# Kernel tuning notes

Measured on AMD Instinct MI355X. Metric: run time of the kernel, lower is better.

The kernel has to match this reference:

```python
import jax, jax.numpy as jnp
import numpy as np

B, L, K, D = 32, 1024, 1024, 1024

def setup_inputs() -> dict:
    key = jax.random.key(0)
    k1, k2, k3, k4, k5 = jax.random.split(key, 5)
    query = jax.random.normal(k1, (B, L, D), dtype=jnp.float32)
    context = jax.random.normal(k2, (B, K, D), dtype=jnp.float32)
    mask = jax.random.randint(k3, (B * L, K), 0, 2, dtype=jnp.int32)
    W_in = jax.random.normal(k4, (D, D), dtype=jnp.float32) * (D ** -0.5)
    W_out = jax.random.normal(k5, (D, 2 * D), dtype=jnp.float32) * ((2 * D) ** -0.5)
    return {"query": query, "context": context, "mask": mask, "W_in": W_in, "W_out": W_out}

def reference(query, context, mask, W_in, W_out):
    b, l, d = query.shape
    k = context.shape[1]
    # linear_in (general attention): q @ W_in.T
    q = jnp.einsum('bld,ed->ble', query, W_in)
    # attention scores [b, l, k]
    scores = jnp.einsum('bld,bkd->blk', q, context)
    # multiplicative-mask softmax with renormalization (masked_softmax, non-memory-efficient path)
    m = mask.astype(scores.dtype).reshape(b, l, k)
    w = jax.nn.softmax(scores * m, axis=-1) * m
    w = w / (jnp.sum(w, axis=-1, keepdims=True) + 1e-13)
    # mix attended context, concat with transformed query, project, tanh
    mix = jnp.einsum('blk,bkd->bld', w, context)
    combined = jnp.concatenate([mix, q], axis=-1)          # [b, l, 2d]
    out = jnp.tanh(jnp.einsum('blc,dc->bld', combined, W_out))
    return out
```

## Files before the change

kernel.cpp:

```cpp
#include <hip/hip_runtime.h>
#include <math.h>

typedef __bf16 bf16_t;
typedef __bf16 bf16x4 __attribute__((ext_vector_type(4)));
typedef __bf16 bf16x8 __attribute__((ext_vector_type(8)));
typedef _Float16 f16x4 __attribute__((ext_vector_type(4)));
typedef _Float16 f16x8 __attribute__((ext_vector_type(8)));
typedef float f32x4 __attribute__((ext_vector_type(4)));
typedef int i32x4 __attribute__((ext_vector_type(4)));

#define MFMA_BF16 __builtin_amdgcn_mfma_f32_16x16x32_bf16
#define MFMA_F16  __builtin_amdgcn_mfma_f32_16x16x32_f16


__device__ __forceinline__ bf16_t to_bf16_rne(float x, float& rep) {
    unsigned u = __builtin_bit_cast(unsigned, x);
    unsigned r = u + 0x7fffu + ((u >> 16) & 1u);
    unsigned short h = (unsigned short)(r >> 16);
    rep = __builtin_bit_cast(float, ((unsigned)h) << 16);
    return __builtin_bit_cast(bf16_t, h);
}

__device__ __forceinline__ void g2l16(const void* g, void* l) {
    __builtin_amdgcn_global_load_lds(
        (const __attribute__((address_space(1))) unsigned int*)g,
        (__attribute__((address_space(3))) unsigned int*)l, 16, 0, 0);
}

__device__ __forceinline__ int lch(int r, int j) {
    return (r * 8 + (j ^ (r & 7))) * 8;
}

template <typename T>
__device__ __forceinline__ void stage2(const T* __restrict__ gA, long long ldA,
                                       const T* __restrict__ gB, long long ldB,
                                       T* buf, int tid) {
    int wid = tid >> 6, lane = tid & 63;
#pragma unroll
    for (int i = 0; i < 4; ++i) {
        int cb = i * 512 + wid * 64;
        int c = cb + lane;
        int r = c >> 3, j = (c & 7) ^ (r & 7);
        g2l16(gA + (long long)r * ldA + j * 8, buf + (size_t)cb * 8);
    }
#pragma unroll
    for (int i = 0; i < 4; ++i) {
        int cb = i * 512 + wid * 64;
        int c = cb + lane;
        int r = c >> 3, j = (c & 7) ^ (r & 7);
        g2l16(gB + (long long)r * ldB + j * 8, buf + 16384 + (size_t)cb * 8);
    }
}


__global__ __launch_bounds__(256) void split_int_k(const float* __restrict__ in,
                                                   bf16_t* __restrict__ out,
                                                   long long n4) {
    long long i = (long long)blockIdx.x * 256 + threadIdx.x;
    if (i >= n4) return;
    f32x4 v = ((const f32x4*)in)[i];
    bf16x4 hv, lv;
#pragma unroll
    for (int j = 0; j < 4; ++j) {
        float rep;
        hv[j] = to_bf16_rne(v[j], rep);
        float res = v[j] - rep;
        float rep2;
        lv[j] = to_bf16_rne(res, rep2);
    }
    long long row = i >> 8;
    int k = (int)(i & 255) * 4;
    long long base = row * 2048 + ((k >> 5) << 6) + (k & 31);
    *(bf16x4*)(out + base) = hv;
    *(bf16x4*)(out + base + 32) = lv;
}

__global__ __launch_bounds__(256) void cast_f16_k(const float* __restrict__ in,
                                                  _Float16* __restrict__ o, long long n4) {
    long long i = (long long)blockIdx.x * 256 + threadIdx.x;
    if (i >= n4) return;
    f32x4 v = ((const f32x4*)in)[i];
    f16x4 h;
#pragma unroll
    for (int j = 0; j < 4; ++j) h[j] = (_Float16)v[j];
    ((f16x4*)o)[i] = h;
}

__global__ __launch_bounds__(256) void prep_ctx_k(const float* __restrict__ ctx,
                                                  bf16_t* __restrict__ ctx_int,
                                                  _Float16* __restrict__ ctxT) {
    __shared__ _Float16 tl[32][33];
    int b = blockIdx.z;
    int k0 = blockIdx.x * 32, d0 = blockIdx.y * 32;
    const float* src = ctx + ((long long)b * 1024 + k0) * 1024 + d0;
    int x = threadIdx.x, y = threadIdx.y;
#pragma unroll
    for (int i = 0; i < 4; ++i) {
        int k = y + i * 8;
        float v = src[(long long)k * 1024 + x];
        float rep;
        bf16_t hb = to_bf16_rne(v, rep);
        float rep2;
        bf16_t lb = to_bf16_rne(v - rep, rep2);
        long long rb = ((long long)b * 1024 + k0 + k) * 2048 + d0 * 2 + x;
        ctx_int[rb] = hb;
        ctx_int[rb + 32] = lb;
        tl[x][k] = (_Float16)v;
    }
    __syncthreads();
    _Float16* dst = ctxT + ((long long)b * 1024 + d0) * 1024 + k0;
#pragma unroll
    for (int i = 0; i < 4; ++i) {
        int dd = y + i * 8;
        dst[(long long)dd * 1024 + x] = tl[dd][x];
    }
}

__global__ __launch_bounds__(256) void masked_softmax_k(const float* __restrict__ s,
                                                        const int* __restrict__ m,
                                                        _Float16* __restrict__ w) {
    long long row = blockIdx.x;
    const f32x4* sr = (const f32x4*)(s + row * 1024);
    const i32x4* mr = (const i32x4*)(m + row * 1024);
    f16x4* wr_ = (f16x4*)(w + row * 1024);
    int t = threadIdx.x;
    int lane = t & 63, wid = t >> 6;
    f32x4 v = sr[t];
    i32x4 mk = mr[t];
    float mx = -3.0e38f;
#pragma unroll
    for (int i = 0; i < 4; ++i)
        if (mk[i]) mx = fmaxf(mx, v[i]);
#pragma unroll
    for (int off = 32; off; off >>= 1) mx = fmaxf(mx, __shfl_xor(mx, off));
    __shared__ float rm[4], rs[4];
    if (!lane) rm[wid] = mx;
    __syncthreads();
    mx = fmaxf(fmaxf(rm[0], rm[1]), fmaxf(rm[2], rm[3]));
    float sum = 0.f;
    f32x4 e;
#pragma unroll
    for (int i = 0; i < 4; ++i) {
        e[i] = mk[i] ? expf(v[i] - mx) : 0.f;
        sum += e[i];
    }
#pragma unroll
    for (int off = 32; off; off >>= 1) sum += __shfl_xor(sum, off);
    if (!lane) rs[wid] = sum;
    __syncthreads();
    sum = rs[0] + rs[1] + rs[2] + rs[3];
    float inv = sum > 0.f ? 1.0f / sum : 0.f;
    f16x4 o;
#pragma unroll
    for (int i = 0; i < 4; ++i) o[i] = (_Float16)(e[i] * inv);
    wr_[t] = o;
}

template <int EPI>
__global__ __launch_bounds__(512, 2) void gemm_x3_256(
    const bf16_t* __restrict__ Aint, const bf16_t* __restrict__ Bint,
    long long sA, long long sB, long long sC, int nbx, int nby,
    float* __restrict__ Cs, bf16_t* __restrict__ Qint, _Float16* __restrict__ Qf) {
    __shared__ bf16_t lds[65536];
    const int NT = 32;
    int tid = threadIdx.x, lane = tid & 63, wid = tid >> 6;
    int wr = wid >> 2, wc = wid & 3;
    int nwg = gridDim.x;
    int bid = blockIdx.x;
    int lid = (bid & 7) * (nwg >> 3) + (bid >> 3);
    int by = lid % nby;
    int t2 = lid / nby;
    int bx = t2 % nbx;
    int z = t2 / nbx;
    const bf16_t* At = Aint + (long long)z * sA + (long long)bx * 256 * 2048;
    const bf16_t* Bt = Bint + (long long)z * sB + (long long)by * 256 * 2048;
    stage2(At, 2048ll, Bt, 2048ll, lds, tid);
    stage2(At + 64, 2048ll, Bt + 64, 2048ll, lds + 32768, tid);
    f32x4 acc[8][4] = {};
    for (int t = 0; t < NT; ++t) {
        bf16_t* buf = lds + (size_t)(t & 1) * 32768;
        bf16_t* bufB = buf + 16384;
        if (t < NT - 1) {
            asm volatile("s_waitcnt vmcnt(8)" ::: "memory");
        } else {
            asm volatile("s_waitcnt vmcnt(0)" ::: "memory");
        }
        __builtin_amdgcn_sched_barrier(0);
        __builtin_amdgcn_s_barrier();
        __builtin_amdgcn_sched_barrier(0);
        bf16x8 bh[4], bl[4];
#pragma unroll
        for (int n = 0; n < 4; ++n) {
            int rB = wc * 64 + n * 16 + (lane & 15);
            bh[n] = *(const bf16x8*)(bufB + lch(rB, lane >> 4));
            bl[n] = *(const bf16x8*)(bufB + lch(rB, 4 + (lane >> 4)));
        }
#pragma unroll
        for (int p = 0; p < 3; ++p) {
            bf16x8 ah[2], al[2];
#pragma unroll
            for (int i = 0; i < 2; ++i) {
                int rA = wr * 128 + (p * 2 + i) * 16 + (lane & 15);
                ah[i] = *(const bf16x8*)(buf + lch(rA, lane >> 4));
                al[i] = *(const bf16x8*)(buf + lch(rA, 4 + (lane >> 4)));
            }
            __builtin_amdgcn_s_setprio(1);
#pragma unroll
            for (int i = 0; i < 2; ++i)
#pragma unroll
                for (int n = 0; n < 4; ++n) {
                    f32x4 a = acc[p * 2 + i][n];
                    a = MFMA_BF16(ah[i], bh[n], a, 0, 0, 0);
                    a = MFMA_BF16(ah[i], bl[n], a, 0, 0, 0);
                    a = MFMA_BF16(al[i], bh[n], a, 0, 0, 0);
                    acc[p * 2 + i][n] = a;
                }
            __builtin_amdgcn_s_setprio(0);
        }
        bf16x8 ah3[2], al3[2];
#pragma unroll
        for (int i = 0; i < 2; ++i) {
            int rA = wr * 128 + (6 + i) * 16 + (lane & 15);
            ah3[i] = *(const bf16x8*)(buf + lch(rA, lane >> 4));
            al3[i] = *(const bf16x8*)(buf + lch(rA, 4 + (lane >> 4)));
        }
        asm volatile("s_waitcnt lgkmcnt(0)" ::: "memory");
        __builtin_amdgcn_sched_barrier(0);
        __builtin_amdgcn_s_barrier();
        __builtin_amdgcn_sched_barrier(0);
        if (t + 2 < NT)
            stage2(At + (long long)(t + 2) * 64, 2048ll, Bt + (long long)(t + 2) * 64,
                   2048ll, buf, tid);
        __builtin_amdgcn_s_setprio(1);
#pragma unroll
        for (int i = 0; i < 2; ++i)
#pragma unroll
            for (int n = 0; n < 4; ++n) {
                f32x4 a = acc[6 + i][n];
                a = MFMA_BF16(ah3[i], bh[n], a, 0, 0, 0);
                a = MFMA_BF16(ah3[i], bl[n], a, 0, 0, 0);
                a = MFMA_BF16(al3[i], bh[n], a, 0, 0, 0);
                acc[6 + i][n] = a;
            }
        __builtin_amdgcn_s_setprio(0);
    }
    int r0 = bx * 256 + wr * 128 + ((lane >> 4) << 2);
    int c0 = by * 256 + wc * 64 + (lane & 15);
#pragma unroll
    for (int m = 0; m < 8; ++m)
#pragma unroll
        for (int n = 0; n < 4; ++n)
#pragma unroll
            for (int j = 0; j < 4; ++j) {
                int r = r0 + m * 16 + j;
                int c = c0 + n * 16;
                float v = acc[m][n][j];
                if (EPI == 0) {
                    Cs[(long long)z * sC + (long long)r * 1024 + c] = v;
                } else {
                    float rep;
                    bf16_t hb = to_bf16_rne(v, rep);
                    float res = v - rep;
                    float rep2;
                    bf16_t lb = to_bf16_rne(res, rep2);
                    long long rb = (long long)r * 2048 + ((c >> 5) << 6) + (c & 31);
                    Qint[rb] = hb;
                    Qint[rb + 32] = lb;
                    Qf[(long long)r * 1024 + c] = (_Float16)v;
                }
            }
}

template <int EPI>
__global__ __launch_bounds__(512, 2) void gemm_f16_256(
    const _Float16* __restrict__ A1, const _Float16* __restrict__ A2,
    const _Float16* __restrict__ B,
    long long ldA, long long ldB, long long sA, long long sB, long long sC,
    int NT, int swt, int nbx, int nby,
    _Float16* __restrict__ Cm, float* __restrict__ Co) {
    __shared__ _Float16 lds[65536];
    int tid = threadIdx.x, lane = tid & 63, wid = tid >> 6;
    int wr = wid >> 2, wc = wid & 3;
    int nwg = gridDim.x;
    int bid = blockIdx.x;
    int lid = (bid & 7) * (nwg >> 3) + (bid >> 3);
    int by = lid % nby;
    int t2 = lid / nby;
    int bx = t2 % nbx;
    int z = t2 / nbx;
    const _Float16* A1t = A1 + (long long)z * sA + (long long)bx * 256 * ldA;
    const _Float16* A2t = A2 + (long long)bx * 256 * ldA;
    const _Float16* Bt = B + (long long)z * sB + (long long)by * 256 * ldB;
    stage2((0 < swt) ? A1t : A2t, ldA, Bt, ldB, lds, tid);
    stage2((1 < swt) ? A1t + 64 : A2t + (long long)(1 - swt) * 64, ldA, Bt + 64, ldB,
           lds + 32768, tid);
    f32x4 acc[8][4] = {};
    for (int t = 0; t < NT; ++t) {
        _Float16* buf = lds + (size_t)(t & 1) * 32768;
        _Float16* bufB = buf + 16384;
        if (t < NT - 1) {
            asm volatile("s_waitcnt vmcnt(8)" ::: "memory");
        } else {
            asm volatile("s_waitcnt vmcnt(0)" ::: "memory");
        }
        __builtin_amdgcn_sched_barrier(0);
        __builtin_amdgcn_s_barrier();
        __builtin_amdgcn_sched_barrier(0);
        f16x8 bfr[4][2];
#pragma unroll
        for (int n = 0; n < 4; ++n)
#pragma unroll
            for (int ks = 0; ks < 2; ++ks) {
                int rB = wc * 64 + n * 16 + (lane & 15);
                bfr[n][ks] = *(const f16x8*)(bufB + lch(rB, ks * 4 + (lane >> 4)));
            }
#pragma unroll
        for (int p = 0; p < 3; ++p) {
            f16x8 a[2][2];
#pragma unroll
            for (int i = 0; i < 2; ++i)
#pragma unroll
                for (int ks = 0; ks < 2; ++ks) {
                    int rA = wr * 128 + (p * 2 + i) * 16 + (lane & 15);
                    a[i][ks] = *(const f16x8*)(buf + lch(rA, ks * 4 + (lane >> 4)));
                }
            __builtin_amdgcn_s_setprio(1);
#pragma unroll
            for (int i = 0; i < 2; ++i)
#pragma unroll
                for (int n = 0; n < 4; ++n) {
                    f32x4 v = acc[p * 2 + i][n];
                    v = MFMA_F16(a[i][0], bfr[n][0], v, 0, 0, 0);
                    v = MFMA_F16(a[i][1], bfr[n][1], v, 0, 0, 0);
                    acc[p * 2 + i][n] = v;
                }
            __builtin_amdgcn_s_setprio(0);
        }
        f16x8 a3[2][2];
#pragma unroll
        for (int i = 0; i < 2; ++i)
#pragma unroll
            for (int ks = 0; ks < 2; ++ks) {
                int rA = wr * 128 + (6 + i) * 16 + (lane & 15);
                a3[i][ks] = *(const f16x8*)(buf + lch(rA, ks * 4 + (lane >> 4)));
            }
        asm volatile("s_waitcnt lgkmcnt(0)" ::: "memory");
        __builtin_amdgcn_sched_barrier(0);
        __builtin_amdgcn_s_barrier();
        __builtin_amdgcn_sched_barrier(0);
        if (t + 2 < NT) {
            int tt = t + 2;
            const _Float16* gA =
                (tt < swt) ? A1t + (long long)tt * 64 : A2t + (long long)(tt - swt) * 64;
            stage2(gA, ldA, Bt + (long long)tt * 64, ldB,
                   lds + (size_t)(tt & 1) * 32768, tid);
        }
        __builtin_amdgcn_s_setprio(1);
#pragma unroll
        for (int i = 0; i < 2; ++i)
#pragma unroll
            for (int n = 0; n < 4; ++n) {
                f32x4 v = acc[6 + i][n];
                v = MFMA_F16(a3[i][0], bfr[n][0], v, 0, 0, 0);
                v = MFMA_F16(a3[i][1], bfr[n][1], v, 0, 0, 0);
                acc[6 + i][n] = v;
            }
        __builtin_amdgcn_s_setprio(0);
    }
    int r0 = bx * 256 + wr * 128 + ((lane >> 4) << 2);
    int c0 = by * 256 + wc * 64 + (lane & 15);
#pragma unroll
    for (int m = 0; m < 8; ++m)
#pragma unroll
        for (int n = 0; n < 4; ++n)
#pragma unroll
            for (int j = 0; j < 4; ++j) {
                int r = r0 + m * 16 + j;
                int c = c0 + n * 16;
                float v = acc[m][n][j];
                if (EPI == 0) {
                    Cm[(long long)z * sC + (long long)r * 1024 + c] = (_Float16)v;
                } else {
                    Co[(long long)r * 1024 + c] = tanhf(v);
                }
            }
}


extern "C" void kernel_launch(void* const* d_in, const int* in_sizes, int n_in,
                              void* d_out, int out_size, void* d_ws, size_t ws_size,
                              hipStream_t stream) {
    const float* query = (const float*)d_in[0];
    const float* ctx = (const float*)d_in[1];
    const int* mask = (const int*)d_in[2];
    const float* Win = (const float*)d_in[3];
    const float* Wout = (const float*)d_in[4];
    float* outp = (float*)d_out;

    const long long MB = 1048576ll;
    int G = 1;
    if ((long long)ws_size >= 512 * MB) G = 32;
    else if ((long long)ws_size >= 256 * MB) G = 16;
    else if ((long long)ws_size >= 128 * MB) G = 8;
    else if ((long long)ws_size >= 64 * MB) G = 4;
    else if ((long long)ws_size >= 32 * MB) G = 2;

    char* p = (char*)d_ws;
    const long long R = (long long)G * 1024;
    bf16_t* qint = (bf16_t*)p; p += 4 * G * MB;
    _Float16* qf = (_Float16*)p; p += 2 * G * MB;
    char* slabA = p; p += 4 * G * MB;
    bf16_t* win_int = (bf16_t*)slabA;
    bf16_t* ctx_int = (bf16_t*)slabA;
    _Float16* wf = (_Float16*)slabA;
    _Float16* mixf = (_Float16*)(slabA + 2 * G * MB);
    _Float16* ctxT = (_Float16*)p; p += 2 * G * MB;
    char* slabC = p;
    bf16_t* qs_int = (bf16_t*)slabC;
    float* scores = (float*)slabC;
    _Float16* woutf = (_Float16*)slabC;

    const long long LD = 1048576ll;

    for (int b0 = 0; b0 < 32; b0 += G) {
        const float* qsrc = query + (long long)b0 * LD;
        const float* csrc = ctx + (long long)b0 * LD;
        split_int_k<<<1024, 256, 0, stream>>>(Win, win_int, 262144ll);
        split_int_k<<<(int)R, 256, 0, stream>>>(qsrc, qs_int, R * 256);
        gemm_x3_256<1><<<16 * G, 512, 0, stream>>>(
            qs_int, win_int, 0, 0, 0, 4 * G, 4, nullptr, qint, qf);
        prep_ctx_k<<<dim3(32, 32, G), dim3(32, 8, 1), 0, stream>>>(csrc, ctx_int, ctxT);
        gemm_x3_256<0><<<16 * G, 512, 0, stream>>>(
            qint, ctx_int, 2097152ll, 2097152ll, 1048576ll, 4, 4,
            scores, nullptr, nullptr);
        masked_softmax_k<<<(int)R, 256, 0, stream>>>(
            scores, mask + (long long)b0 * 1024 * 1024, wf);
        cast_f16_k<<<2048, 256, 0, stream>>>(Wout, woutf, 524288ll);
        gemm_f16_256<0><<<16 * G, 512, 0, stream>>>(
            wf, wf, ctxT, 1024ll, 1024ll, 1048576ll, 1048576ll, 1048576ll,
            16, 1 << 20, 4, 4, mixf, nullptr);
        gemm_f16_256<1><<<16 * G, 512, 0, stream>>>(
            mixf, qf, woutf, 1024ll, 2048ll, 0, 0, 0,
            32, 16, 4 * G, 4, nullptr, outp + (long long)b0 * LD);
    }
}
```

Measured before the change: 778.8 us.

## Restructure GEMM main loops into barrier-fenced phases with split A/B prefetch

Result: faster. 762.3 us (median of 2 runs) (-2.1%).

```diff
diff --git a/kernel.cpp b/kernel.cpp
--- a/kernel.cpp
+++ b/kernel.cpp
@@ -12,6 +12,17 @@
 #define MFMA_BF16 __builtin_amdgcn_mfma_f32_16x16x32_bf16
 #define MFMA_F16  __builtin_amdgcn_mfma_f32_16x16x32_f16
 
+#define P_PRE                                         \
+    __builtin_amdgcn_sched_barrier(0);                \
+    __builtin_amdgcn_s_barrier();                     \
+    asm volatile("s_waitcnt lgkmcnt(0)" ::: "memory");\
+    __builtin_amdgcn_sched_barrier(0);                \
+    __builtin_amdgcn_s_setprio(1)
+#define P_POST                                        \
+    __builtin_amdgcn_s_setprio(0);                    \
+    __builtin_amdgcn_sched_barrier(0);                \
+    __builtin_amdgcn_s_barrier()
+
 
 __device__ __forceinline__ bf16_t to_bf16_rne(float x, float& rep) {
     unsigned u = __builtin_bit_cast(unsigned, x);
@@ -32,9 +43,8 @@
 }
 
 template <typename T>
-__device__ __forceinline__ void stage2(const T* __restrict__ gA, long long ldA,
-                                       const T* __restrict__ gB, long long ldB,
-                                       T* buf, int tid) {
+__device__ __forceinline__ void stageA4(const T* __restrict__ gA, long long ldA,
+                                        T* buf, int tid) {
     int wid = tid >> 6, lane = tid & 63;
 #pragma unroll
     for (int i = 0; i < 4; ++i) {
@@ -43,6 +53,12 @@
         int r = c >> 3, j = (c & 7) ^ (r & 7);
         g2l16(gA + (long long)r * ldA + j * 8, buf + (size_t)cb * 8);
     }
+}
+
+template <typename T>
+__device__ __forceinline__ void stageB4(const T* __restrict__ gB, long long ldB,
+                                        T* buf, int tid) {
+    int wid = tid >> 6, lane = tid & 63;
 #pragma unroll
     for (int i = 0; i < 4; ++i) {
         int cb = i * 512 + wid * 64;
@@ -50,6 +66,14 @@
         int r = c >> 3, j = (c & 7) ^ (r & 7);
         g2l16(gB + (long long)r * ldB + j * 8, buf + 16384 + (size_t)cb * 8);
     }
+}
+
+template <typename T>
+__device__ __forceinline__ void stage2(const T* __restrict__ gA, long long ldA,
+                                       const T* __restrict__ gB, long long ldB,
+                                       T* buf, int tid) {
+    stageA4(gA, ldA, buf, tid);
+    stageB4(gB, ldB, buf, tid);
 }
 
 
@@ -169,83 +193,118 @@
     int bid = blockIdx.x;
     int lid = (bid & 7) * (nwg >> 3) + (bid >> 3);
     int by = lid % nby;
-    int t2 = lid / nby;
-    int bx = t2 % nbx;
-    int z = t2 / nbx;
+    int t2_ = lid / nby;
+    int bx = t2_ % nbx;
+    int z = t2_ / nbx;
     const bf16_t* At = Aint + (long long)z * sA + (long long)bx * 256 * 2048;
     const bf16_t* Bt = Bint + (long long)z * sB + (long long)by * 256 * 2048;
     stage2(At, 2048ll, Bt, 2048ll, lds, tid);
     stage2(At + 64, 2048ll, Bt + 64, 2048ll, lds + 32768, tid);
     f32x4 acc[8][4] = {};
+    int l15 = lane & 15, l4 = lane >> 4;
+    asm volatile("s_waitcnt vmcnt(8)" ::: "memory");
+    __builtin_amdgcn_sched_barrier(0);
+    __builtin_amdgcn_s_barrier();
     for (int t = 0; t < NT; ++t) {
         bf16_t* buf = lds + (size_t)(t & 1) * 32768;
         bf16_t* bufB = buf + 16384;
-        if (t < NT - 1) {
+        const bf16_t* At2 = At + (long long)(t + 2) * 64;
+        const bf16_t* Bt2 = Bt + (long long)(t + 2) * 64;
+        bool st = (t + 2 < NT);
+        bf16x8 bh[4], bl[4], ahA[2], alA[2];
+#pragma unroll
+        for (int n = 0; n < 4; ++n) {
+            int rB = wc * 64 + n * 16 + l15;
+            bh[n] = *(const bf16x8*)(bufB + lch(rB, l4));
+            bl[n] = *(const bf16x8*)(bufB + lch(rB, 4 + l4));
+        }
+#pragma unroll
+        for (int i = 0; i < 2; ++i) {
+            int rA = wr * 128 + i * 16 + l15;
+            ahA[i] = *(const bf16x8*)(buf + lch(rA, l4));
+            alA[i] = *(const bf16x8*)(buf + lch(rA, 4 + l4));
+        }
+        P_PRE;
+#pragma unroll
+        for (int i = 0; i < 2; ++i)
+#pragma unroll
+            for (int n = 0; n < 4; ++n) {
+                f32x4 a = acc[i][n];
+                a = MFMA_BF16(ahA[i], bh[n], a, 0, 0, 0);
+                a = MFMA_BF16(ahA[i], bl[n], a, 0, 0, 0);
+                a = MFMA_BF16(alA[i], bh[n], a, 0, 0, 0);
+                acc[i][n] = a;
+            }
+        P_POST;
+        bf16x8 ahB[2], alB[2], ahC[2], alC[2];
+#pragma unroll
+        for (int i = 0; i < 2; ++i) {
+            int rA = wr * 128 + (2 + i) * 16 + l15;
+            ahB[i] = *(const bf16x8*)(buf + lch(rA, l4));
+            alB[i] = *(const bf16x8*)(buf + lch(rA, 4 + l4));
+        }
+#pragma unroll
+        for (int i = 0; i < 2; ++i) {
+            int rA = wr * 128 + (4 + i) * 16 + l15;
+            ahC[i] = *(const bf16x8*)(buf + lch(rA, l4));
+            alC[i] = *(const bf16x8*)(buf + lch(rA, 4 + l4));
+        }
+        P_PRE;
+#pragma unroll
+        for (int i = 0; i < 2; ++i)
+#pragma unroll
+            for (int n = 0; n < 4; ++n) {
+                f32x4 a = acc[2 + i][n];
+                a = MFMA_BF16(ahB[i], bh[n], a, 0, 0, 0);
+                a = MFMA_BF16(ahB[i], bl[n], a, 0, 0, 0);
+                a = MFMA_BF16(alB[i], bh[n], a, 0, 0, 0);
+                acc[2 + i][n] = a;
+            }
+        P_POST;
+        bf16x8 ahD[2], alD[2];
+#pragma unroll
+        for (int i = 0; i < 2; ++i) {
+            int rA = wr * 128 + (6 + i) * 16 + l15;
+            ahD[i] = *(const bf16x8*)(buf + lch(rA, l4));
+            alD[i] = *(const bf16x8*)(buf + lch(rA, 4 + l4));
+        }
+        if (st) stageB4(Bt2, 2048ll, buf, tid);
+        P_PRE;
+#pragma unroll
+        for (int i = 0; i < 2; ++i)
+#pragma unroll
+            for (int n = 0; n < 4; ++n) {
+                f32x4 a = acc[4 + i][n];
+                a = MFMA_BF16(ahC[i], bh[n], a, 0, 0, 0);
+                a = MFMA_BF16(ahC[i], bl[n], a, 0, 0, 0);
+                a = MFMA_BF16(alC[i], bh[n], a, 0, 0, 0);
+                acc[4 + i][n] = a;
+            }
+        P_POST;
+        if (st) stageA4(At2, 2048ll, buf, tid);
+        __builtin_amdgcn_s_setprio(1);
+#pragma unroll
+        for (int i = 0; i < 2; ++i)
+#pragma unroll
+            for (int n = 0; n < 4; ++n) {
+                f32x4 a = acc[6 + i][n];
+                a = MFMA_BF16(ahD[i], bh[n], a, 0, 0, 0);
+                a = MFMA_BF16(ahD[i], bl[n], a, 0, 0, 0);
+                a = MFMA_BF16(alD[i], bh[n], a, 0, 0, 0);
+                acc[6 + i][n] = a;
+            }
+        __builtin_amdgcn_s_setprio(0);
+        __builtin_amdgcn_sched_barrier(0);
+        if (t + 2 < NT) {
             asm volatile("s_waitcnt vmcnt(8)" ::: "memory");
-        } else {
+        } else if (t + 1 < NT) {
             asm volatile("s_waitcnt vmcnt(0)" ::: "memory");
         }
         __builtin_amdgcn_sched_barrier(0);
         __builtin_amdgcn_s_barrier();
-        __builtin_amdgcn_sched_barrier(0);
-        bf16x8 bh[4], bl[4];
-#pragma unroll
-        for (int n = 0; n < 4; ++n) {
-            int rB = wc * 64 + n * 16 + (lane & 15);
-            bh[n] = *(const bf16x8*)(bufB + lch(rB, lane >> 4));
-            bl[n] = *(const bf16x8*)(bufB + lch(rB, 4 + (lane >> 4)));
-        }
-#pragma unroll
-        for (int p = 0; p < 3; ++p) {
-            bf16x8 ah[2], al[2];
-#pragma unroll
-            for (int i = 0; i < 2; ++i) {
-                int rA = wr * 128 + (p * 2 + i) * 16 + (lane & 15);
-                ah[i] = *(const bf16x8*)(buf + lch(rA, lane >> 4));
-                al[i] = *(const bf16x8*)(buf + lch(rA, 4 + (lane >> 4)));
-            }
-            __builtin_amdgcn_s_setprio(1);
-#pragma unroll
-            for (int i = 0; i < 2; ++i)
-#pragma unroll
-                for (int n = 0; n < 4; ++n) {
-                    f32x4 a = acc[p * 2 + i][n];
-                    a = MFMA_BF16(ah[i], bh[n], a, 0, 0, 0);
-                    a = MFMA_BF16(ah[i], bl[n], a, 0, 0, 0);
-                    a = MFMA_BF16(al[i], bh[n], a, 0, 0, 0);
-                    acc[p * 2 + i][n] = a;
-                }
-            __builtin_amdgcn_s_setprio(0);
-        }
-        bf16x8 ah3[2], al3[2];
-#pragma unroll
-        for (int i = 0; i < 2; ++i) {
-            int rA = wr * 128 + (6 + i) * 16 + (lane & 15);
-            ah3[i] = *(const bf16x8*)(buf + lch(rA, lane >> 4));
-            al3[i] = *(const bf16x8*)(buf + lch(rA, 4 + (lane >> 4)));
-        }
-        asm volatile("s_waitcnt lgkmcnt(0)" ::: "memory");
-        __builtin_amdgcn_sched_barrier(0);
-        __builtin_amdgcn_s_barrier();
-        __builtin_amdgcn_sched_barrier(0);
-        if (t + 2 < NT)
-            stage2(At + (long long)(t + 2) * 64, 2048ll, Bt + (long long)(t + 2) * 64,
-                   2048ll, buf, tid);
-        __builtin_amdgcn_s_setprio(1);
-#pragma unroll
-        for (int i = 0; i < 2; ++i)
-#pragma unroll
-            for (int n = 0; n < 4; ++n) {
-                f32x4 a = acc[6 + i][n];
-                a = MFMA_BF16(ah3[i], bh[n], a, 0, 0, 0);
-                a = MFMA_BF16(ah3[i], bl[n], a, 0, 0, 0);
-                a = MFMA_BF16(al3[i], bh[n], a, 0, 0, 0);
-                acc[6 + i][n] = a;
-            }
-        __builtin_amdgcn_s_setprio(0);
-    }
-    int r0 = bx * 256 + wr * 128 + ((lane >> 4) << 2);
-    int c0 = by * 256 + wc * 64 + (lane & 15);
+    }
+    int r0 = bx * 256 + wr * 128 + (l4 << 2);
+    int c0 = by * 256 + wc * 64 + l15;
 #pragma unroll
     for (int m = 0; m < 8; ++m)
 #pragma unroll
@@ -285,9 +344,9 @@
     int bid = blockIdx.x;
     int lid = (bid & 7) * (nwg >> 3) + (bid >> 3);
     int by = lid % nby;
-    int t2 = lid / nby;
-    int bx = t2 % nbx;
-    int z = t2 / nbx;
+    int t2_ = lid / nby;
+    int bx = t2_ % nbx;
+    int z = t2_ / nbx;
     const _Float16* A1t = A1 + (long long)z * sA + (long long)bx * 256 * ldA;
     const _Float16* A2t = A2 + (long long)bx * 256 * ldA;
     const _Float16* Bt = B + (long long)z * sB + (long long)by * 256 * ldB;
@@ -295,80 +354,113 @@
     stage2((1 < swt) ? A1t + 64 : A2t + (long long)(1 - swt) * 64, ldA, Bt + 64, ldB,
            lds + 32768, tid);
     f32x4 acc[8][4] = {};
+    int l15 = lane & 15, l4 = lane >> 4;
+    asm volatile("s_waitcnt vmcnt(8)" ::: "memory");
+    __builtin_amdgcn_sched_barrier(0);
+    __builtin_amdgcn_s_barrier();
     for (int t = 0; t < NT; ++t) {
         _Float16* buf = lds + (size_t)(t & 1) * 32768;
         _Float16* bufB = buf + 16384;
-        if (t < NT - 1) {
+        int tt = t + 2;
+        bool st = (tt < NT);
+        const _Float16* gA2 =
+            (tt < swt) ? A1t + (long long)tt * 64 : A2t + (long long)(tt - swt) * 64;
+        const _Float16* gB2 = Bt + (long long)tt * 64;
+        f16x8 bfr[4][2], aA[2][2];
+#pragma unroll
+        for (int n = 0; n < 4; ++n) {
+            int rB = wc * 64 + n * 16 + l15;
+#pragma unroll
+            for (int ks = 0; ks < 2; ++ks)
+                bfr[n][ks] = *(const f16x8*)(bufB + lch(rB, ks * 4 + l4));
+        }
+#pragma unroll
+        for (int i = 0; i < 2; ++i) {
+            int rA = wr * 128 + i * 16 + l15;
+#pragma unroll
+            for (int ks = 0; ks < 2; ++ks)
+                aA[i][ks] = *(const f16x8*)(buf + lch(rA, ks * 4 + l4));
+        }
+        P_PRE;
+#pragma unroll
+        for (int i = 0; i < 2; ++i)
+#pragma unroll
+            for (int n = 0; n < 4; ++n) {
+                f32x4 v = acc[i][n];
+                v = MFMA_F16(aA[i][0], bfr[n][0], v, 0, 0, 0);
+                v = MFMA_F16(aA[i][1], bfr[n][1], v, 0, 0, 0);
+                acc[i][n] = v;
+            }
+        P_POST;
+        f16x8 aB[2][2], aC[2][2];
+#pragma unroll
+        for (int i = 0; i < 2; ++i) {
+            int rA = wr * 128 + (2 + i) * 16 + l15;
+#pragma unroll
+            for (int ks = 0; ks < 2; ++ks)
+                aB[i][ks] = *(const f16x8*)(buf + lch(rA, ks * 4 + l4));
+        }
+#pragma unroll
+        for (int i = 0; i < 2; ++i) {
+            int rA = wr * 128 + (4 + i) * 16 + l15;
+#pragma unroll
+            for (int ks = 0; ks < 2; ++ks)
+                aC[i][ks] = *(const f16x8*)(buf + lch(rA, ks * 4 + l4));
+        }
+        P_PRE;
+#pragma unroll
+        for (int i = 0; i < 2; ++i)
+#pragma unroll
+            for (int n = 0; n < 4; ++n) {
+                f32x4 v = acc[2 + i][n];
+                v = MFMA_F16(aB[i][0], bfr[n][0], v, 0, 0, 0);
+                v = MFMA_F16(aB[i][1], bfr[n][1], v, 0, 0, 0);
+                acc[2 + i][n] = v;
+            }
+        P_POST;
+        f16x8 aD[2][2];
+#pragma unroll
+        for (int i = 0; i < 2; ++i) {
+            int rA = wr * 128 + (6 + i) * 16 + l15;
+#pragma unroll
+            for (int ks = 0; ks < 2; ++ks)
+                aD[i][ks] = *(const f16x8*)(buf + lch(rA, ks * 4 + l4));
+        }
+        if (st) stageB4(gB2, ldB, buf, tid);
+        P_PRE;
+#pragma unroll
+        for (int i = 0; i < 2; ++i)
+#pragma unroll
+            for (int n = 0; n < 4; ++n) {
+                f32x4 v = acc[4 + i][n];
+                v = MFMA_F16(aC[i][0], bfr[n][0], v, 0, 0, 0);
+                v = MFMA_F16(aC[i][1], bfr[n][1], v, 0, 0, 0);
+                acc[4 + i][n] = v;
+            }
+        P_POST;
+        if (st) stageA4(gA2, ldA, buf, tid);
+        __builtin_amdgcn_s_setprio(1);
+#pragma unroll
+        for (int i = 0; i < 2; ++i)
+#pragma unroll
+            for (int n = 0; n < 4; ++n) {
+                f32x4 v = acc[6 + i][n];
+                v = MFMA_F16(aD[i][0], bfr[n][0], v, 0, 0, 0);
+                v = MFMA_F16(aD[i][1], bfr[n][1], v, 0, 0, 0);
+                acc[6 + i][n] = v;
+            }
+        __builtin_amdgcn_s_setprio(0);
+        __builtin_amdgcn_sched_barrier(0);
+        if (t + 2 < NT) {
             asm volatile("s_waitcnt vmcnt(8)" ::: "memory");
-        } else {
+        } else if (t + 1 < NT) {
             asm volatile("s_waitcnt vmcnt(0)" ::: "memory");
         }
         __builtin_amdgcn_sched_barrier(0);
         __builtin_amdgcn_s_barrier();
-        __builtin_amdgcn_sched_barrier(0);
-        f16x8 bfr[4][2];
-#pragma unroll
-        for (int n = 0; n < 4; ++n)
-#pragma unroll
-            for (int ks = 0; ks < 2; ++ks) {
-                int rB = wc * 64 + n * 16 + (lane & 15);
-                bfr[n][ks] = *(const f16x8*)(bufB + lch(rB, ks * 4 + (lane >> 4)));
-            }
-#pragma unroll
-        for (int p = 0; p < 3; ++p) {
-            f16x8 a[2][2];
-#pragma unroll
-            for (int i = 0; i < 2; ++i)
-#pragma unroll
-                for (int ks = 0; ks < 2; ++ks) {
-                    int rA = wr * 128 + (p * 2 + i) * 16 + (lane & 15);
-                    a[i][ks] = *(const f16x8*)(buf + lch(rA, ks * 4 + (lane >> 4)));
-                }
-            __builtin_amdgcn_s_setprio(1);
-#pragma unroll
-            for (int i = 0; i < 2; ++i)
-#pragma unroll
-                for (int n = 0; n < 4; ++n) {
-                    f32x4 v = acc[p * 2 + i][n];
-                    v = MFMA_F16(a[i][0], bfr[n][0], v, 0, 0, 0);
-                    v = MFMA_F16(a[i][1], bfr[n][1], v, 0, 0, 0);
-                    acc[p * 2 + i][n] = v;
-                }
-            __builtin_amdgcn_s_setprio(0);
-        }
-        f16x8 a3[2][2];
-#pragma unroll
-        for (int i = 0; i < 2; ++i)
-#pragma unroll
-            for (int ks = 0; ks < 2; ++ks) {
-                int rA = wr * 128 + (6 + i) * 16 + (lane & 15);
-                a3[i][ks] = *(const f16x8*)(buf + lch(rA, ks * 4 + (lane >> 4)));
-            }
-        asm volatile("s_waitcnt lgkmcnt(0)" ::: "memory");
-        __builtin_amdgcn_sched_barrier(0);
-        __builtin_amdgcn_s_barrier();
-        __builtin_amdgcn_sched_barrier(0);
-        if (t + 2 < NT) {
-            int tt = t + 2;
-            const _Float16* gA =
-                (tt < swt) ? A1t + (long long)tt * 64 : A2t + (long long)(tt - swt) * 64;
-            stage2(gA, ldA, Bt + (long long)tt * 64, ldB,
-                   lds + (size_t)(tt & 1) * 32768, tid);
-        }
-        __builtin_amdgcn_s_setprio(1);
-#pragma unroll
-        for (int i = 0; i < 2; ++i)
-#pragma unroll
-            for (int n = 0; n < 4; ++n) {
-                f32x4 v = acc[6 + i][n];
-                v = MFMA_F16(a3[i][0], bfr[n][0], v, 0, 0, 0);
-                v = MFMA_F16(a3[i][1], bfr[n][1], v, 0, 0, 0);
-                acc[6 + i][n] = v;
-            }
-        __builtin_amdgcn_s_setprio(0);
-    }
-    int r0 = bx * 256 + wr * 128 + ((lane >> 4) << 2);
-    int c0 = by * 256 + wc * 64 + (lane & 15);
+    }
+    int r0 = bx * 256 + wr * 128 + (l4 << 2);
+    int c0 = by * 256 + wc * 64 + l15;
 #pragma unroll
     for (int m = 0; m < 8; ++m)
 #pragma unroll
```
